# Performance work log

Measured on AMD Instinct MI355X. Metric: run time of the kernel, lower is better.

Reference implementation:

```python
import jax, jax.numpy as jnp
import numpy as np

B, N, D, P = 128, 6, 256, 5
DS = 32                      # attention downsize channels
TEMP = (DS * P * P) ** 0.5   # sqrt(800)
EPS = 1e-6


def conv2d(x, w, b):
    # x: [n, Cin, P, P], w: [Cout, Cin, kh, kw] (3x3 pad1 or 1x1) -> SAME
    y = jax.lax.conv_general_dilated(x, w, (1, 1), 'SAME',
                                     dimension_numbers=('NCHW', 'OIHW', 'NCHW'))
    return y + b[None, :, None, None]


def layer_norm(x, g, b):
    # nn.LayerNorm([N, D, P, P]) on [B, N, D, P, P]: normalize over last 4 dims
    mu = x.mean(axis=(1, 2, 3, 4), keepdims=True)
    var = x.var(axis=(1, 2, 3, 4), keepdims=True)
    return (x - mu) / jnp.sqrt(var + EPS) * g[None] + b[None]


def setup_inputs():
    key = jax.random.key(0)
    ks = jax.random.split(key, 12)
    sc = 0.05
    x = jax.random.normal(ks[0], (B, N, D, P, P), jnp.float32)
    valid = jnp.ones((B, N), jnp.float32)
    # all ordered object pairs (i, j), j != i, with pair-valid flag 1
    pairs = np.array([[i, j, 1] for i in range(N) for j in range(N) if j != i], np.int64)
    g_idx = jnp.asarray(np.broadcast_to(pairs[None], (B, N * (N - 1), 3)).copy())
    self_w = jax.random.normal(ks[1], (D, D, 3, 3), jnp.float32) * sc
    self_b = jnp.zeros((D,), jnp.float32)
    rel_w = jax.random.normal(ks[2], (D, 2 * D, 3, 3), jnp.float32) * sc
    rel_b = jnp.zeros((D,), jnp.float32)
    aff_w = jax.random.normal(ks[3], (D, D, 3, 3), jnp.float32) * sc
    aff_b = jnp.zeros((D,), jnp.float32)
    attn_w = jax.random.normal(ks[4], (DS, D, 1, 1), jnp.float32) * sc
    attn_b = jnp.zeros((DS,), jnp.float32)
    wq = jax.random.normal(ks[5], (DS * P * P, DS * P * P), jnp.float32) * sc
    wk = wq  # tie q/k so attn diagonal = ||q||^2/T > 0, guaranteeing a finite softmax row
    aggt_w = jax.random.normal(ks[6], (D, D, 3, 3), jnp.float32) * sc
    aggt_b = jnp.zeros((D,), jnp.float32)
    ff_w = jax.random.normal(ks[7], (D * P * P, D * P * P), jnp.float32) * 0.01
    ln_aff_g = jnp.ones((N, D, P, P), jnp.float32); ln_aff_b = jnp.zeros((N, D, P, P), jnp.float32)
    ln1_g = jnp.ones((N, D, P, P), jnp.float32); ln1_b = jnp.zeros((N, D, P, P), jnp.float32)
    ln2_g = jnp.ones((N, D, P, P), jnp.float32); ln2_b = jnp.zeros((N, D, P, P), jnp.float32)
    return dict(x=x, valid=valid, g_idx=g_idx, self_w=self_w, self_b=self_b,
                rel_w=rel_w, rel_b=rel_b, aff_w=aff_w, aff_b=aff_b,
                attn_w=attn_w, attn_b=attn_b, wq=wq, wk=wk,
                aggt_w=aggt_w, aggt_b=aggt_b, ff_w=ff_w,
                ln_aff_g=ln_aff_g, ln_aff_b=ln_aff_b,
                ln1_g=ln1_g, ln1_b=ln1_b, ln2_g=ln2_g, ln2_b=ln2_b)


_OFF_COLS = np.array([[j for j in range(N) if j != i] for i in range(N)])  # [N, N-1]
_ROWS = np.arange(N)[:, None]


def reference(x, valid, g_idx, self_w, self_b, rel_w, rel_b, aff_w, aff_b,
              attn_w, attn_b, wq, wk, aggt_w, aggt_b, ff_w,
              ln_aff_g, ln_aff_b, ln1_g, ln1_b, ln2_g, ln2_b):
    s = x
    Bq = x.shape[0]
    bi = jnp.arange(Bq)[:, None]
    # pairwise relation construction via gather into (N-1)-tiled object axis
    x1 = jnp.tile(x, (1, N - 1, 1, 1, 1))            # [B, N(N-1), D, P, P]
    y1 = x1[bi, g_idx[:, :, 0]]
    y2 = x1[bi, g_idx[:, :, 1]]
    r = jnp.concatenate([y1, y2], axis=2) * g_idx[:, :, 2][:, :, None, None, None].astype(x.dtype)
    r = jax.nn.relu(conv2d(r.reshape(-1, 2 * D, P, P), rel_w, rel_b))
    r = r.reshape(Bq, N, N - 1, D, P, P)
    # masked self/rel attention over objects
    s2d = conv2d(s.reshape(-1, D, P, P), attn_w, attn_b).reshape(-1, DS * P * P)
    q = (s2d @ wq.T).reshape(Bq, N, -1)
    k = (s2d @ wk.T).reshape(Bq, N, -1)
    attn = jnp.einsum('bnd,bmd->bnm', q / TEMP, k)
    attn_m = attn * valid[:, None, :]
    attn_m = jnp.where(attn_m > 0, attn_m, -jnp.inf)  # clamp non-positive to -inf
    sm = jax.nn.softmax(attn_m, axis=-1) * N
    self_wts = jnp.diagonal(sm, axis1=1, axis2=2)                 # [B, N]
    rel_wts = sm[:, _ROWS, _OFF_COLS]                             # [B, N, N-1] off-diagonal
    r = rel_wts[:, :, :, None, None, None] * r + r
    r = r.sum(axis=2)                                             # [B, N, D, P, P]
    xs = jax.nn.relu(conv2d(x.reshape(-1, D, P, P), self_w, self_b)).reshape(Bq, N, D, P, P)
    pred = self_wts[:, :, None, None, None] * xs + r
    a = jax.nn.relu(conv2d(pred.reshape(-1, D, P, P), aff_w, aff_b)).reshape(Bq, N, D, P, P)
    a = layer_norm(a, ln_aff_g, ln_aff_b)
    # trans=True branch
    a = layer_norm(a + s, ln1_g, ln1_b)
    z = jax.nn.relu(conv2d(a.reshape(-1, D, P, P), aggt_w, aggt_b)).reshape(Bq, N, D, P, P)
    ff = (z.reshape(-1, D * P * P) @ ff_w.T).reshape(Bq, N, D, P, P)
    out = layer_norm(ff + z, ln2_g, ln2_b)
    return out
```

## Files before the change

kernel.cpp:

```cpp
#include <hip/hip_runtime.h>
#include <hip/hip_bf16.h>
#include <math.h>

#define Bq 128
#define Nn 6
#define Dc 256
#define PP 25
#define SAMP 768
#define CHW 6400
#define SAMPLE_F 38400
#define QKD 800
#define KTOT 2304
#define CROW 264
#define CSAMP (26*CROW)
#define TS 2
#define NT 4

typedef short bf16x8 __attribute__((ext_vector_type(8)));
typedef float f32x4 __attribute__((ext_vector_type(4)));

__device__ __forceinline__ short f2b(float f) {
  unsigned u = __float_as_uint(f);
  unsigned r = (u + 0x7FFFu + ((u >> 16) & 1u)) >> 16;
  return (short)r;
}
__device__ __forceinline__ float b2f(short s) {
  return __uint_as_float(((unsigned)(unsigned short)s) << 16);
}
__device__ __forceinline__ int pack2(short a, short b) {
  return (int)(((unsigned)(unsigned short)a) | (((unsigned)(unsigned short)b) << 16));
}
__device__ __forceinline__ void b8f(const int4 v, float* f) {
  unsigned x0 = (unsigned)v.x, x1 = (unsigned)v.y;
  unsigned x2 = (unsigned)v.z, x3 = (unsigned)v.w;
  f[0] = __uint_as_float(x0 << 16); f[1] = __uint_as_float(x0 & 0xffff0000u);
  f[2] = __uint_as_float(x1 << 16); f[3] = __uint_as_float(x1 & 0xffff0000u);
  f[4] = __uint_as_float(x2 << 16); f[5] = __uint_as_float(x2 & 0xffff0000u);
  f[6] = __uint_as_float(x3 << 16); f[7] = __uint_as_float(x3 & 0xffff0000u);
}

__global__ __launch_bounds__(256) void k_repack5(const float* __restrict__ self_w,
    const float* __restrict__ rel_w, const float* __restrict__ aff_w,
    const float* __restrict__ aggt_w, short* __restrict__ WbAll) {
  int z = blockIdx.y;
  int idx = blockIdx.x * 256 + threadIdx.x;
  const float* W; int stride, cioff;
  if (z == 0)      { W = self_w; stride = 2304; cioff = 0; }
  else if (z == 1) { W = rel_w;  stride = 4608; cioff = 0; }
  else if (z == 2) { W = rel_w;  stride = 4608; cioff = 256; }
  else if (z == 3) { W = aff_w;  stride = 2304; cioff = 0; }
  else             { W = aggt_w; stride = 2304; cioff = 0; }
  int chunk = idx >> 9;
  int within = idx & 511;
  int l = within >> 3, i = within & 7;
  int ct = chunk / 72, rem = chunk - ct * 72;
  int tap = rem >> 3, kb = rem & 7;
  int co = ct * 16 + (l & 15);
  int ci = kb * 32 + (l >> 4) * 8 + i;
  WbAll[(size_t)z * (Dc * KTOT) + idx] =
      f2b(W[(size_t)co * stride + (size_t)(cioff + ci) * 9 + tap]);
}

__global__ __launch_bounds__(256) void k_cvtw(const float* __restrict__ in,
    short* __restrict__ out) {
  size_t i = ((size_t)blockIdx.x * 256 + threadIdx.x) * 8;
  float4 a = *(const float4*)(in + i);
  float4 b = *(const float4*)(in + i + 4);
  int4 o;
  o.x = pack2(f2b(a.x), f2b(a.y));
  o.y = pack2(f2b(a.z), f2b(a.w));
  o.z = pack2(f2b(b.x), f2b(b.y));
  o.w = pack2(f2b(b.z), f2b(b.w));
  *(int4*)(out + i) = o;
}

__global__ __launch_bounds__(256) void k_s2dx(const float* __restrict__ x,
    const float* __restrict__ attn_w, const float* __restrict__ attn_b,
    float* __restrict__ s2d, short* __restrict__ XT) {
  __shared__ float xs[CHW];
  __shared__ short lt[25 * CROW];
  int row = blockIdx.x;
  int t = threadIdx.x;
  const float* xr = x + (size_t)row * CHW;
  for (int i = t; i < CHW; i += 256) xs[i] = xr[i];
  __syncthreads();
  for (int e = t; e < CHW; e += 256) {
    int ci = e / 25, pq = e - ci * 25;
    lt[pq * CROW + ci] = f2b(xs[e]);
  }
  for (int o = t; o < QKD; o += 256) {
    int c = o / PP, pq = o % PP;
    float acc = attn_b[c];
    const float* wr = attn_w + c * Dc;
    for (int ci = 0; ci < Dc; ++ci) acc += wr[ci] * xs[ci * PP + pq];
    s2d[(size_t)row * QKD + o] = acc;
  }
  __syncthreads();
  short* ob = XT + (size_t)row * CHW;
  for (int c = t; c < 800; c += 256) {
    int pix = c >> 5, ch = c & 31;
    *(int4*)(ob + pix * 256 + ch * 8) = *(const int4*)(lt + pix * CROW + ch * 8);
  }
}

__global__ __launch_bounds__(512) void k_split3b(const float* __restrict__ inA,
    short* __restrict__ plA, const float* __restrict__ inB,
    short* __restrict__ plB) {
  int z = blockIdx.y;
  const float* in = z ? inB : inA;
  short* pl = z ? plB : plA;
  int T = z ? 56 : 48;
  int R = z ? QKD : SAMP;
  int tile = blockIdx.x / 25, kb = blockIdx.x % 25;
  if (tile >= T) return;
  int t = threadIdx.x;
  int l = t >> 3, i = t & 7;
  int row = tile * 16 + (l & 15);
  int k = kb * 32 + (l >> 4) * 8 + i;
  float x = (row < R) ? in[(size_t)row * QKD + k] : 0.f;
  short h = f2b(x);
  float r1 = x - b2f(h);
  short m = f2b(r1);
  float r2 = r1 - b2f(m);
  short lo = f2b(r2);
  size_t PT = (size_t)T * 25 * 512;
  size_t off = ((size_t)tile * 25 + kb) * 512 + t;
  pl[off] = h;
  pl[PT + off] = m;
  pl[2 * PT + off] = lo;
}

__global__ __launch_bounds__(512) void k_qgemm(const short* __restrict__ Ap,
    const short* __restrict__ Bp, float* __restrict__ qp) {
  int t = threadIdx.x;
  int nT = blockIdx.x, mT = blockIdx.y, kz = blockIdx.z;
  int lane = t & 63, wv = t >> 6;
  int wm = wv >> 2, wn = wv & 3;
  int col = lane & 15, kg = lane >> 4;
  const size_t PTA = (size_t)48 * 25 * 512;
  const size_t PTB = (size_t)56 * 25 * 512;

  f32x4 acc[4][2] = {};
#pragma unroll
  for (int kk = 0; kk < 5; ++kk) {
    int kb = kz * 5 + kk;
    bf16x8 bh[2], bm[2], bl[2];
#pragma unroll
    for (int nt = 0; nt < 2; ++nt) {
      size_t off = ((size_t)(nT * 8 + wn * 2 + nt) * 25 + kb) * 512 + lane * 8;
      bh[nt] = *(const bf16x8*)(Bp + off);
      bm[nt] = *(const bf16x8*)(Bp + PTB + off);
      bl[nt] = *(const bf16x8*)(Bp + 2 * PTB + off);
    }
#pragma unroll
    for (int mt = 0; mt < 4; ++mt) {
      size_t off = ((size_t)(mT * 8 + wm * 4 + mt) * 25 + kb) * 512 + lane * 8;
      bf16x8 ah = *(const bf16x8*)(Ap + off);
      bf16x8 am = *(const bf16x8*)(Ap + PTA + off);
      bf16x8 al = *(const bf16x8*)(Ap + 2 * PTA + off);
#pragma unroll
      for (int nt = 0; nt < 2; ++nt) {
        acc[mt][nt] = __builtin_amdgcn_mfma_f32_16x16x32_bf16(ah, bh[nt], acc[mt][nt], 0, 0, 0);
        acc[mt][nt] = __builtin_amdgcn_mfma_f32_16x16x32_bf16(ah, bm[nt], acc[mt][nt], 0, 0, 0);
        acc[mt][nt] = __builtin_amdgcn_mfma_f32_16x16x32_bf16(am, bh[nt], acc[mt][nt], 0, 0, 0);
        acc[mt][nt] = __builtin_amdgcn_mfma_f32_16x16x32_bf16(ah, bl[nt], acc[mt][nt], 0, 0, 0);
        acc[mt][nt] = __builtin_amdgcn_mfma_f32_16x16x32_bf16(al, bh[nt], acc[mt][nt], 0, 0, 0);
        acc[mt][nt] = __builtin_amdgcn_mfma_f32_16x16x32_bf16(am, bm[nt], acc[mt][nt], 0, 0, 0);
      }
    }
  }
  float* Q = qp + (size_t)kz * SAMP * QKD;
#pragma unroll
  for (int mt = 0; mt < 4; ++mt) {
    int gr = mT * 128 + wm * 64 + mt * 16 + kg * 4;
#pragma unroll
    for (int nt = 0; nt < 2; ++nt) {
      int gc = nT * 128 + wn * 32 + nt * 16 + col;
      if (gc >= QKD) continue;
#pragma unroll
      for (int r = 0; r < 4; ++r)
        Q[(size_t)(gr + r) * QKD + gc] = acc[mt][nt][r];
    }
  }
}

__global__ __launch_bounds__(256) void k_attn5(const float* __restrict__ qp,
    const float* __restrict__ valid, float* __restrict__ sm) {
  __shared__ float q[6 * QKD];
  __shared__ float at[36];
  int b = blockIdx.x, t = threadIdx.x;
  size_t base = (size_t)b * 6 * QKD;
  const size_t PS = (size_t)SAMP * QKD;
  for (int i = t; i < 6 * QKD; i += 256) {
    q[i] = qp[base + i] + qp[PS + base + i] + qp[2 * PS + base + i]
         + qp[3 * PS + base + i] + qp[4 * PS + base + i];
  }
  __syncthreads();
  if (t < 36) {
    int n = t / 6, m = t % 6;
    const float4* qn = (const float4*)&q[n * QKD];
    const float4* qm = (const float4*)&q[m * QKD];
    float acc = 0.f;
    for (int d = 0; d < QKD / 4; ++d) {
      float4 a = qn[d], c = qm[d];
      acc += a.x * c.x + a.y * c.y + a.z * c.z + a.w * c.w;
    }
    at[t] = acc * 0.035355339059327376f * valid[b * 6 + m];
  }
  __syncthreads();
  if (t < 6) {
    float v[6]; float mx = -1e30f;
#pragma unroll
    for (int m = 0; m < 6; ++m) {
      float a = at[t * 6 + m];
      v[m] = (a > 0.f) ? a : -1e30f;
      mx = fmaxf(mx, v[m]);
    }
    float e[6]; float se = 0.f;
#pragma unroll
    for (int m = 0; m < 6; ++m) { e[m] = expf(v[m] - mx); se += e[m]; }
    float sc = 6.f / se;
#pragma unroll
    for (int m = 0; m < 6; ++m) sm[(size_t)b * 36 + t * 6 + m] = e[m] * sc;
  }
}

__global__ __launch_bounds__(256) void k_convT(const short* __restrict__ XT,
    const short* __restrict__ WbBase, float* __restrict__ YBase,
    const float* __restrict__ bias, short* __restrict__ Ybf,
    size_t wStride, size_t yStride) {
  __shared__ __align__(16) short xpt[TS * CSAMP];
  int t = threadIdx.x;
  int s0 = blockIdx.x * TS;
  int z = blockIdx.y;
  const short* Wb = WbBase + (size_t)z * wStride;
  float* Y = YBase ? (YBase + (size_t)z * yStride) : nullptr;
  int hasBR = (z == 0);

  if (t < TS * 33) {
    int smp = t / 33, i4 = t - smp * 33;
    *(int4*)(xpt + smp * CSAMP + 25 * CROW + i4 * 8) = int4{0, 0, 0, 0};
  }
  for (int c = t; c < TS * 800; c += 256) {
    int smp = c / 800, rem = c - smp * 800;
    int pix = rem >> 5, ch = rem & 31;
    *(int4*)(xpt + smp * CSAMP + pix * CROW + ch * 8) =
        *(const int4*)(XT + ((size_t)(s0 + smp) * 25 + pix) * 256 + ch * 8);
  }
  __syncthreads();

  int lane = t & 63, wv = t >> 6;
  int col = lane & 15, kg = lane >> 4;
  int cobase = wv * 64;
  const short* wtile[4];
#pragma unroll
  for (int mt = 0; mt < 4; ++mt)
    wtile[mt] = Wb + ((size_t)(wv * 4 + mt) * 72) * 512 + lane * 8;
  int o0 = col, o1 = col + 16;
  int orow0 = o0 / 5, ocol0 = o0 - orow0 * 5;
  int orow1 = o1 / 5, ocol1 = o1 - orow1 * 5;

  bf16x8 wA[4], wB[4];
#pragma unroll
  for (int mt = 0; mt < 4; ++mt) wA[mt] = *(const bf16x8*)(wtile[mt]);
#pragma unroll
  for (int mt = 0; mt < 4; ++mt) wB[mt] = *(const bf16x8*)(wtile[mt] + 512);

  f32x4 acc[4][NT] = {};
  for (int tap = 0; tap < 9; ++tap) {
    int dh = tap / 3 - 1, dw = tap % 3 - 1;
    int pb[NT];
#pragma unroll
    for (int nt = 0; nt < NT; ++nt) {
      int hi = nt & 1;
      int irow = (hi ? orow1 : orow0) + dh;
      int icol = (hi ? ocol1 : ocol0) + dw;
      bool good = ((unsigned)irow < 5u) && ((unsigned)icol < 5u) &&
                  (hi ? (o1 < 25) : true);
      int pix = good ? irow * 5 + icol : 25;
      pb[nt] = (nt >> 1) * CSAMP + pix * CROW + kg * 8;
    }
#pragma unroll
    for (int kb2 = 0; kb2 < 4; ++kb2) {
      int it = tap * 8 + kb2 * 2;
      {
        int kb = kb2 * 2;
        bf16x8 bfr[NT];
#pragma unroll
        for (int nt = 0; nt < NT; ++nt)
          bfr[nt] = *(const bf16x8*)(xpt + pb[nt] + kb * 32);
#pragma unroll
        for (int mt = 0; mt < 4; ++mt)
#pragma unroll
          for (int nt = 0; nt < NT; ++nt)
            acc[mt][nt] = __builtin_amdgcn_mfma_f32_16x16x32_bf16(wA[mt], bfr[nt], acc[mt][nt], 0, 0, 0);
      }
      if (it + 2 < 72) {
#pragma unroll
        for (int mt = 0; mt < 4; ++mt)
          wA[mt] = *(const bf16x8*)(wtile[mt] + (size_t)(it + 2) * 512);
      }
      {
        int kb = kb2 * 2 + 1;
        bf16x8 bfr[NT];
#pragma unroll
        for (int nt = 0; nt < NT; ++nt)
          bfr[nt] = *(const bf16x8*)(xpt + pb[nt] + kb * 32);
#pragma unroll
        for (int mt = 0; mt < 4; ++mt)
#pragma unroll
          for (int nt = 0; nt < NT; ++nt)
            acc[mt][nt] = __builtin_amdgcn_mfma_f32_16x16x32_bf16(wB[mt], bfr[nt], acc[mt][nt], 0, 0, 0);
      }
      if (it + 3 < 72) {
#pragma unroll
        for (int mt = 0; mt < 4; ++mt)
          wB[mt] = *(const bf16x8*)(wtile[mt] + (size_t)(it + 3) * 512);
      }
    }
  }
#pragma unroll
  for (int mt = 0; mt < 4; ++mt) {
    int co = cobase + mt * 16 + kg * 4;
    float bb[4];
#pragma unroll
    for (int r = 0; r < 4; ++r) bb[r] = hasBR ? bias[co + r] : 0.f;
#pragma unroll
    for (int nt = 0; nt < NT; ++nt) {
      int o = (nt & 1) * 16 + col;
      if (o >= 25) continue;
      size_t sbase = (size_t)(s0 + (nt >> 1)) * CHW + o;
#pragma unroll
      for (int r = 0; r < 4; ++r) {
        float v = acc[mt][nt][r] + bb[r];
        if (hasBR) v = fmaxf(v, 0.f);
        if (Y) Y[sbase + (size_t)(co + r) * PP] = v;
        if (Ybf) Ybf[sbase + (size_t)(co + r) * PP] = f2b(v);
      }
    }
  }
}

__global__ __launch_bounds__(256) void k_combineT(const float* __restrict__ xs,
    const float* __restrict__ cA, const float* __restrict__ cB,
    const float* __restrict__ sm, const float* __restrict__ rel_b,
    short* __restrict__ predT) {
  __shared__ short lt[25 * CROW];
  int s = blockIdx.x;
  int b = s / 6, i = s % 6;
  const float* smb = sm + (size_t)b * 36;
  float wself = smb[6 * i + i];
  float wr[5]; int js[5];
#pragma unroll
  for (int jj = 0; jj < 5; ++jj) {
    int j = jj + (jj >= i ? 1 : 0);
    js[jj] = j;
    wr[jj] = smb[6 * i + j] + 1.f;
  }
  size_t base = (size_t)s * CHW;
  size_t bbase = (size_t)b * 6 * CHW;
  for (int e = threadIdx.x; e < CHW; e += 256) {
    int ci = e / PP, pq = e - ci * PP;
    float rb = rel_b[ci];
    float av = cA[base + e];
    float acc = wself * xs[base + e];
#pragma unroll
    for (int jj = 0; jj < 5; ++jj) {
      float bvv = cB[bbase + (size_t)js[jj] * CHW + e];
      float rv = av + bvv + rb;
      rv = rv > 0.f ? rv : 0.f;
      acc = fmaf(wr[jj], rv, acc);
    }
    lt[pq * CROW + ci] = f2b(acc);
  }
  __syncthreads();
  short* ob = predT + (size_t)s * CHW;
  for (int c = threadIdx.x; c < 800; c += 256) {
    int pix = c >> 5, ch = c & 31;
    *(int4*)(ob + pix * 256 + ch * 8) = *(const int4*)(lt + pix * CROW + ch * 8);
  }
}

__global__ __launch_bounds__(256) void k_ln(const float* __restrict__ in1,
    const float* __restrict__ in1b, const float* __restrict__ in2,
    const float* __restrict__ g, const float* __restrict__ beta,
    float* __restrict__ out) {
  int b = blockIdx.x;
  int t = threadIdx.x;
  const float2* p1 = (const float2*)(in1 + (size_t)b * SAMPLE_F);
  const float2* p1b = in1b ? (const float2*)(in1b + (size_t)b * SAMPLE_F) : nullptr;
  const float2* p2 = in2 ? (const float2*)(in2 + (size_t)b * SAMPLE_F) : nullptr;
  float s = 0.f, s2 = 0.f;
  for (int i = t; i < SAMPLE_F / 2; i += 256) {
    float2 v = p1[i];
    if (p1b) { float2 w = p1b[i]; v.x += w.x; v.y += w.y; }
    if (p2) { float2 w = p2[i]; v.x += w.x; v.y += w.y; }
    s += v.x + v.y;
    s2 += v.x * v.x + v.y * v.y;
  }
#pragma unroll
  for (int off = 32; off >= 1; off >>= 1) {
    s += __shfl_xor(s, off);
    s2 += __shfl_xor(s2, off);
  }
  __shared__ float rs[4], rs2[4];
  int w = t >> 6;
  if ((t & 63) == 0) { rs[w] = s; rs2[w] = s2; }
  __syncthreads();
  float S = rs[0] + rs[1] + rs[2] + rs[3];
  float S2 = rs2[0] + rs2[1] + rs2[2] + rs2[3];
  const float inv_n = 1.f / (float)SAMPLE_F;
  float mean = S * inv_n;
  float var = S2 * inv_n - mean * mean;
  float rstd = 1.f / sqrtf(var + 1e-6f);
  const float2* gp = (const float2*)g;
  const float2* bp = (const float2*)beta;
  float2* op = (float2*)(out + (size_t)b * SAMPLE_F);
  for (int i = t; i < SAMPLE_F / 2; i += 256) {
    float2 v = p1[i];
    if (p1b) { float2 w = p1b[i]; v.x += w.x; v.y += w.y; }
    if (p2) { float2 w2 = p2[i]; v.x += w2.x; v.y += w2.y; }
    float2 gv = gp[i], bvv = bp[i];
    float2 o;
    o.x = (v.x - mean) * rstd * gv.x + bvv.x;
    o.y = (v.y - mean) * rstd * gv.y + bvv.y;
    op[i] = o;
  }
}

__global__ __launch_bounds__(256) void k_lnF2(const short* __restrict__ c0,
    const short* __restrict__ c1, const short* __restrict__ c2,
    const short* __restrict__ c3, const short* __restrict__ z,
    const float* __restrict__ g, const float* __restrict__ beta,
    float* __restrict__ out) {
  int b = blockIdx.x;
  int t = threadIdx.x;
  size_t base = (size_t)b * SAMPLE_F;
  float s = 0.f, s2 = 0.f;
  for (int i = t; i < SAMPLE_F / 8; i += 256) {
    float f0[8], f1[8], f2[8], f3[8], fz[8];
    b8f(*(const int4*)(c0 + base + i * 8), f0);
    b8f(*(const int4*)(c1 + base + i * 8), f1);
    b8f(*(const int4*)(c2 + base + i * 8), f2);
    b8f(*(const int4*)(c3 + base + i * 8), f3);
    b8f(*(const int4*)(z  + base + i * 8), fz);
#pragma unroll
    for (int j = 0; j < 8; ++j) {
      float v = f0[j] + f1[j] + f2[j] + f3[j] + fz[j];
      s += v; s2 += v * v;
    }
  }
#pragma unroll
  for (int off = 32; off >= 1; off >>= 1) {
    s += __shfl_xor(s, off);
    s2 += __shfl_xor(s2, off);
  }
  __shared__ float rs[4], rs2[4];
  int w = t >> 6;
  if ((t & 63) == 0) { rs[w] = s; rs2[w] = s2; }
  __syncthreads();
  float S = rs[0] + rs[1] + rs[2] + rs[3];
  float S2 = rs2[0] + rs2[1] + rs2[2] + rs2[3];
  const float inv_n = 1.f / (float)SAMPLE_F;
  float mean = S * inv_n;
  float var = S2 * inv_n - mean * mean;
  float rstd = 1.f / sqrtf(var + 1e-6f);
  for (int i = t; i < SAMPLE_F / 8; i += 256) {
    float f0[8], f1[8], f2[8], f3[8], fz[8];
    b8f(*(const int4*)(c0 + base + i * 8), f0);
    b8f(*(const int4*)(c1 + base + i * 8), f1);
    b8f(*(const int4*)(c2 + base + i * 8), f2);
    b8f(*(const int4*)(c3 + base + i * 8), f3);
    b8f(*(const int4*)(z  + base + i * 8), fz);
    float4 ga = *(const float4*)(g + i * 8);
    float4 gb = *(const float4*)(g + i * 8 + 4);
    float4 ba = *(const float4*)(beta + i * 8);
    float4 bb = *(const float4*)(beta + i * 8 + 4);
    float gg[8] = {ga.x, ga.y, ga.z, ga.w, gb.x, gb.y, gb.z, gb.w};
    float bt[8] = {ba.x, ba.y, ba.z, ba.w, bb.x, bb.y, bb.z, bb.w};
    float o[8];
#pragma unroll
    for (int j = 0; j < 8; ++j) {
      float v = f0[j] + f1[j] + f2[j] + f3[j] + fz[j];
      o[j] = (v - mean) * rstd * gg[j] + bt[j];
    }
    *(float4*)(out + base + i * 8) = *(float4*)&o[0];
    *(float4*)(out + base + i * 8 + 4) = *(float4*)&o[4];
  }
}

__global__ __launch_bounds__(256) void k_lnT(const float* __restrict__ in1,
    const float* __restrict__ in2, const float* __restrict__ g,
    const float* __restrict__ beta, short* __restrict__ outT) {
  __shared__ short lt[25 * CROW];
  __shared__ float rs[4], rs2[4];
  int b = blockIdx.x;
  int t = threadIdx.x;
  const float2* p1 = (const float2*)(in1 + (size_t)b * SAMPLE_F);
  const float2* p2 = (const float2*)(in2 + (size_t)b * SAMPLE_F);
  float s = 0.f, s2 = 0.f;
  for (int i = t; i < SAMPLE_F / 2; i += 256) {
    float2 v = p1[i];
    float2 w = p2[i]; v.x += w.x; v.y += w.y;
    s += v.x + v.y;
    s2 += v.x * v.x + v.y * v.y;
  }
#pragma unroll
  for (int off = 32; off >= 1; off >>= 1) {
    s += __shfl_xor(s, off);
    s2 += __shfl_xor(s2, off);
  }
  int w = t >> 6;
  if ((t & 63) == 0) { rs[w] = s; rs2[w] = s2; }
  __syncthreads();
  float S = rs[0] + rs[1] + rs[2] + rs[3];
  float S2 = rs2[0] + rs2[1] + rs2[2] + rs2[3];
  const float inv_n = 1.f / (float)SAMPLE_F;
  float mean = S * inv_n;
  float var = S2 * inv_n - mean * mean;
  float rstd = 1.f / sqrtf(var + 1e-6f);
  const float* i1 = in1 + (size_t)b * SAMPLE_F;
  const float* i2 = in2 + (size_t)b * SAMPLE_F;
  for (int smp = 0; smp < 6; ++smp) {
    int off0 = smp * CHW;
    for (int e = t; e < CHW; e += 256) {
      int idx = off0 + e;
      float v = i1[idx] + i2[idx];
      v = (v - mean) * rstd * g[idx] + beta[idx];
      int ci = e / PP, pq = e - ci * PP;
      lt[pq * CROW + ci] = f2b(v);
    }
    __syncthreads();
    short* ob = outT + (size_t)(b * 6 + smp) * CHW;
    for (int c = t; c < 800; c += 256) {
      int pix = c >> 5, ch = c & 31;
      *(int4*)(ob + pix * 256 + ch * 8) = *(const int4*)(lt + pix * CROW + ch * 8);
    }
    __syncthreads();
  }
}

__global__ __launch_bounds__(512) void k_ffgemm7(const short* __restrict__ A,
    const short* __restrict__ Bb, short* __restrict__ C0, short* __restrict__ C1,
    short* __restrict__ C2, short* __restrict__ C3) {
  __shared__ __align__(16) short As[128 * 64];
  __shared__ __align__(16) short Bs[128 * 64];
  int t = threadIdx.x;
  int orig = blockIdx.x;
  int swz = (orig & 7) * 150 + (orig >> 3);
  int m = swz % 6;
  int kz = (swz / 6) & 3;
  int n = swz / 24;
  int m0 = m * 128, n0 = n * 128;
  int lane = t & 63, wv = t >> 6;
  int wm = wv >> 2, wn = wv & 3;
  int col = lane & 15, kg = lane >> 4;
  int ra0 = t >> 3, ca0 = t & 7;
  int ra1 = ra0 + 64;

  int4 pa0, pa1, pb0, pb1;
  auto LOADR = [&](int ks) {
    int k0 = (kz * 25 + ks) * 64;
    pa0 = *(const int4*)(A + (size_t)(m0 + ra0) * CHW + k0 + ca0 * 8);
    pa1 = *(const int4*)(A + (size_t)(m0 + ra1) * CHW + k0 + ca0 * 8);
    pb0 = *(const int4*)(Bb + (size_t)(n0 + ra0) * CHW + k0 + ca0 * 8);
    pb1 = *(const int4*)(Bb + (size_t)(n0 + ra1) * CHW + k0 + ca0 * 8);
  };
  auto STORE = [&]() {
    *(int4*)(As + ra0 * 64 + ((ca0 ^ (ra0 & 7)) * 8)) = pa0;
    *(int4*)(As + ra1 * 64 + ((ca0 ^ (ra1 & 7)) * 8)) = pa1;
    *(int4*)(Bs + ra0 * 64 + ((ca0 ^ (ra0 & 7)) * 8)) = pb0;
    *(int4*)(Bs + ra1 * 64 + ((ca0 ^ (ra1 & 7)) * 8)) = pb1;
  };

  f32x4 acc[4][2] = {};
  LOADR(0);
  for (int ks = 0; ks < 25; ++ks) {
    STORE();
    __syncthreads();
    if (ks < 24) LOADR(ks + 1);
#pragma unroll
    for (int s = 0; s < 2; ++s) {
      bf16x8 af[4], bfr[2];
#pragma unroll
      for (int mt = 0; mt < 4; ++mt) {
        int r = wm * 64 + mt * 16 + col;
        af[mt] = *(const bf16x8*)(As + r * 64 + (((s * 4 + kg) ^ (r & 7)) * 8));
      }
#pragma unroll
      for (int nt = 0; nt < 2; ++nt) {
        int r = wn * 32 + nt * 16 + col;
        bfr[nt] = *(const bf16x8*)(Bs + r * 64 + (((s * 4 + kg) ^ (r & 7)) * 8));
      }
#pragma unroll
      for (int mt = 0; mt < 4; ++mt)
#pragma unroll
        for (int nt = 0; nt < 2; ++nt)
          acc[mt][nt] = __builtin_amdgcn_mfma_f32_16x16x32_bf16(af[mt], bfr[nt], acc[mt][nt], 0, 0, 0);
    }
    __syncthreads();
  }
  short* C = (kz == 0) ? C0 : (kz == 1) ? C1 : (kz == 2) ? C2 : C3;
#pragma unroll
  for (int mt = 0; mt < 4; ++mt) {
    int gr = m0 + wm * 64 + mt * 16 + kg * 4;
#pragma unroll
    for (int nt = 0; nt < 2; ++nt) {
      int gc = n0 + wn * 32 + nt * 16 + col;
#pragma unroll
      for (int r = 0; r < 4; ++r)
        C[(size_t)(gr + r) * CHW + gc] = f2b(acc[mt][nt][r]);
    }
  }
}

extern "C" void kernel_launch(void* const* d_in, const int* in_sizes, int n_in,
                              void* d_out, int out_size, void* d_ws, size_t ws_size,
                              hipStream_t stream) {
  const float* x        = (const float*)d_in[0];
  const float* valid    = (const float*)d_in[1];
  const float* self_w   = (const float*)d_in[3];
  const float* self_b   = (const float*)d_in[4];
  const float* rel_w    = (const float*)d_in[5];
  const float* rel_b    = (const float*)d_in[6];
  const float* aff_w    = (const float*)d_in[7];
  const float* aff_b    = (const float*)d_in[8];
  const float* attn_w   = (const float*)d_in[9];
  const float* attn_b   = (const float*)d_in[10];
  const float* wq       = (const float*)d_in[11];
  const float* aggt_w   = (const float*)d_in[13];
  const float* aggt_b   = (const float*)d_in[14];
  const float* ff_w     = (const float*)d_in[15];
  const float* ln_aff_g = (const float*)d_in[16];
  const float* ln_aff_b = (const float*)d_in[17];
  const float* ln1_g    = (const float*)d_in[18];
  const float* ln1_b    = (const float*)d_in[19];
  const float* ln2_g    = (const float*)d_in[20];
  const float* ln2_b    = (const float*)d_in[21];

  float* ws = (float*)d_ws;
  const size_t S = (size_t)SAMP * CHW;
  float* big0 = ws;
  float* big1 = ws + S;
  float* big2 = ws + 2 * S;
  float* regD = ws + 3 * S;
  float* s2d  = regD;
  short* WbAll = (short*)regD;
  float* smb  = regD + 1474560;
  float* fbase = regD + 1474560 + 4608;
  short* Tbuf = (short*)fbase;
  short* spA  = Tbuf + 4915200;
  short* spB  = spA + 1843200;
  float* qp   = (float*)(spB + 2150400);
  short* Wffb = Tbuf;
  short* zb = (short*)big0;
  short* C0 = (short*)big1;
  short* C1 = C0 + S;
  short* C2 = (short*)big2;
  short* C3 = C2 + S;
  float* outp = (float*)d_out;

  const size_t WBSZ = (size_t)Dc * KTOT;

  k_s2dx<<<SAMP, 256, 0, stream>>>(x, attn_w, attn_b, s2d, Tbuf);
  dim3 gs(56 * 25, 2);
  k_split3b<<<gs, 512, 0, stream>>>(s2d, spA, wq, spB);
  dim3 gq(7, 6, 5);
  k_qgemm<<<gq, 512, 0, stream>>>(spA, spB, qp);
  k_attn5<<<Bq, 256, 0, stream>>>(qp, valid, smb);

  dim3 grp(2304, 5);
  k_repack5<<<grp, 256, 0, stream>>>(self_w, rel_w, aff_w, aggt_w, WbAll);

  dim3 gc3(SAMP / TS, 3);
  k_convT<<<gc3, 256, 0, stream>>>(Tbuf, WbAll, big0, self_b, nullptr, WBSZ, S);

  k_combineT<<<SAMP, 256, 0, stream>>>(big0, big1, big2, smb, rel_b, Tbuf);

  dim3 gc1(SAMP / TS, 1);
  k_convT<<<gc1, 256, 0, stream>>>(Tbuf, WbAll + 3 * WBSZ, big0, aff_b, nullptr, 0, 0);
  k_ln<<<Bq, 256, 0, stream>>>(big0, nullptr, nullptr, ln_aff_g, ln_aff_b, big1);
  k_lnT<<<Bq, 256, 0, stream>>>(big1, x, ln1_g, ln1_b, Tbuf);

  k_convT<<<gc1, 256, 0, stream>>>(Tbuf, WbAll + 4 * WBSZ, nullptr, aggt_b, zb, 0, 0);
  k_cvtw<<<20000, 256, 0, stream>>>(ff_w, Wffb);
  k_ffgemm7<<<1200, 512, 0, stream>>>(zb, Wffb, C0, C1, C2, C3);
  k_lnF2<<<Bq, 256, 0, stream>>>(C0, C1, C2, C3, zb, ln2_g, ln2_b, outp);
}
```

Before: 536.7 us.

## Switch conv implicit GEMM to 32x32x16 MFMA with new weight packing

Weight repacking now builds 32-channel by 16-input tiles, and the conv kernel uses 32x32x16 bf16 MFMA instructions. Each wave now handles one sample's 25 pixels (padded to 32) against 128 output channels, in place of 64 channels across both samples with four 16-wide tiles. This cuts the number of MFMA issues and LDS fragment loads per wave and gives more work per instruction. In exchange, 7 of the 32 pixel columns are wasted padding, each wave loads weights for twice as many channels, and the 16-wide accumulators raise register pressure.

```diff
diff --git a/kernel.cpp b/kernel.cpp
--- a/kernel.cpp
+++ b/kernel.cpp
@@ -14,10 +14,10 @@
 #define CROW 264
 #define CSAMP (26*CROW)
 #define TS 2
-#define NT 4
 
 typedef short bf16x8 __attribute__((ext_vector_type(8)));
 typedef float f32x4 __attribute__((ext_vector_type(4)));
+typedef float f32x16 __attribute__((ext_vector_type(16)));
 
 __device__ __forceinline__ short f2b(float f) {
   unsigned u = __float_as_uint(f);
@@ -53,10 +53,10 @@
   int chunk = idx >> 9;
   int within = idx & 511;
   int l = within >> 3, i = within & 7;
-  int ct = chunk / 72, rem = chunk - ct * 72;
-  int tap = rem >> 3, kb = rem & 7;
-  int co = ct * 16 + (l & 15);
-  int ci = kb * 32 + (l >> 4) * 8 + i;
+  int ct = chunk / 144, rem = chunk - ct * 144;
+  int tap = rem >> 4, k16 = rem & 15;
+  int co = ct * 32 + (l & 31);
+  int ci = k16 * 16 + (l >> 5) * 8 + i;
   WbAll[(size_t)z * (Dc * KTOT) + idx] =
       f2b(W[(size_t)co * stride + (size_t)(cioff + ci) * 9 + tap]);
 }
@@ -250,15 +250,15 @@
   __syncthreads();
 
   int lane = t & 63, wv = t >> 6;
-  int col = lane & 15, kg = lane >> 4;
-  int cobase = wv * 64;
+  int smp = wv & 1, cohalf = wv >> 1;
+  int o = lane & 31;
+  int klo = (lane >> 5) * 8;
+  int pbk = smp * CSAMP + klo;
+  int orow = o / 5, ocol = o - orow * 5;
   const short* wtile[4];
 #pragma unroll
   for (int mt = 0; mt < 4; ++mt)
-    wtile[mt] = Wb + ((size_t)(wv * 4 + mt) * 72) * 512 + lane * 8;
-  int o0 = col, o1 = col + 16;
-  int orow0 = o0 / 5, ocol0 = o0 - orow0 * 5;
-  int orow1 = o1 / 5, ocol1 = o1 - orow1 * 5;
+    wtile[mt] = Wb + ((size_t)(cohalf * 4 + mt) * 144) * 512 + lane * 8;
 
   bf16x8 wA[4], wB[4];
 #pragma unroll
@@ -266,76 +266,54 @@
 #pragma unroll
   for (int mt = 0; mt < 4; ++mt) wB[mt] = *(const bf16x8*)(wtile[mt] + 512);
 
-  f32x4 acc[4][NT] = {};
+  f32x16 acc[4] = {};
   for (int tap = 0; tap < 9; ++tap) {
     int dh = tap / 3 - 1, dw = tap % 3 - 1;
-    int pb[NT];
-#pragma unroll
-    for (int nt = 0; nt < NT; ++nt) {
-      int hi = nt & 1;
-      int irow = (hi ? orow1 : orow0) + dh;
-      int icol = (hi ? ocol1 : ocol0) + dw;
-      bool good = ((unsigned)irow < 5u) && ((unsigned)icol < 5u) &&
-                  (hi ? (o1 < 25) : true);
-      int pix = good ? irow * 5 + icol : 25;
-      pb[nt] = (nt >> 1) * CSAMP + pix * CROW + kg * 8;
-    }
-#pragma unroll
-    for (int kb2 = 0; kb2 < 4; ++kb2) {
-      int it = tap * 8 + kb2 * 2;
+    int irow = orow + dh, icol = ocol + dw;
+    bool good = (o < 25) && ((unsigned)irow < 5u) && ((unsigned)icol < 5u);
+    int pix = good ? irow * 5 + icol : 25;
+    int pb = pbk + pix * CROW;
+#pragma unroll
+    for (int k2 = 0; k2 < 8; ++k2) {
+      int it = tap * 16 + k2 * 2;
       {
-        int kb = kb2 * 2;
-        bf16x8 bfr[NT];
-#pragma unroll
-        for (int nt = 0; nt < NT; ++nt)
-          bfr[nt] = *(const bf16x8*)(xpt + pb[nt] + kb * 32);
+        bf16x8 bfr = *(const bf16x8*)(xpt + pb + (k2 * 2) * 16);
 #pragma unroll
         for (int mt = 0; mt < 4; ++mt)
-#pragma unroll
-          for (int nt = 0; nt < NT; ++nt)
-            acc[mt][nt] = __builtin_amdgcn_mfma_f32_16x16x32_bf16(wA[mt], bfr[nt], acc[mt][nt], 0, 0, 0);
-      }
-      if (it + 2 < 72) {
+          acc[mt] = __builtin_amdgcn_mfma_f32_32x32x16_bf16(wA[mt], bfr, acc[mt], 0, 0, 0);
+      }
+      if (it + 2 < 144) {
 #pragma unroll
         for (int mt = 0; mt < 4; ++mt)
           wA[mt] = *(const bf16x8*)(wtile[mt] + (size_t)(it + 2) * 512);
       }
       {
-        int kb = kb2 * 2 + 1;
-        bf16x8 bfr[NT];
-#pragma unroll
-        for (int nt = 0; nt < NT; ++nt)
-          bfr[nt] = *(const bf16x8*)(xpt + pb[nt] + kb * 32);
+        bf16x8 bfr = *(const bf16x8*)(xpt + pb + (k2 * 2 + 1) * 16);
 #pragma unroll
         for (int mt = 0; mt < 4; ++mt)
-#pragma unroll
-          for (int nt = 0; nt < NT; ++nt)
-            acc[mt][nt] = __builtin_amdgcn_mfma_f32_16x16x32_bf16(wB[mt], bfr[nt], acc[mt][nt], 0, 0, 0);
-      }
-      if (it + 3 < 72) {
+          acc[mt] = __builtin_amdgcn_mfma_f32_32x32x16_bf16(wB[mt], bfr, acc[mt], 0, 0, 0);
+      }
+      if (it + 3 < 144) {
 #pragma unroll
         for (int mt = 0; mt < 4; ++mt)
           wB[mt] = *(const bf16x8*)(wtile[mt] + (size_t)(it + 3) * 512);
       }
     }
   }
+  size_t sC = (size_t)(s0 + smp) * CHW;
+  bool pvalid = (o < 25);
+  int rbase = (lane >> 5) * 4;
 #pragma unroll
   for (int mt = 0; mt < 4; ++mt) {
-    int co = cobase + mt * 16 + kg * 4;
-    float bb[4];
-#pragma unroll
-    for (int r = 0; r < 4; ++r) bb[r] = hasBR ? bias[co + r] : 0.f;
-#pragma unroll
-    for (int nt = 0; nt < NT; ++nt) {
-      int o = (nt & 1) * 16 + col;
-      if (o >= 25) continue;
-      size_t sbase = (size_t)(s0 + (nt >> 1)) * CHW + o;
-#pragma unroll
-      for (int r = 0; r < 4; ++r) {
-        float v = acc[mt][nt][r] + bb[r];
-        if (hasBR) v = fmaxf(v, 0.f);
-        if (Y) Y[sbase + (size_t)(co + r) * PP] = v;
-        if (Ybf) Ybf[sbase + (size_t)(co + r) * PP] = f2b(v);
+    int cb = cohalf * 128 + mt * 32;
+#pragma unroll
+    for (int r = 0; r < 16; ++r) {
+      int co = cb + rbase + ((r >> 2) << 3) + (r & 3);
+      float v = acc[mt][r] + (hasBR ? bias[co] : 0.f);
+      if (hasBR) v = fmaxf(v, 0.f);
+      if (pvalid) {
+        if (Y) Y[sC + (size_t)co * PP + o] = v;
+        if (Ybf) Ybf[sC + (size_t)co * PP + o] = f2b(v);
       }
     }
   }
```

Measured after the change: 702.6 us. +30.9%, slower.
